# Kernel tuning notes

Hardware: AMD Instinct MI355X
Metric: run time of the kernel (lower is better)

## Reference

```python
import jax, jax.numpy as jnp
import numpy as np

N_NODES, N_GRAPHS, PER_GRAPH, N_EDGES = 20000, 200, 100, 320000
X_DIM, E_DIM, G_DIM = 32, 16, 32
NUM_EMB, HEADS, LAYERS = 64, 2, 3
EPS_GEN, EPS_LN = 1e-7, 1e-5


def _w(k, shape, scale=0.05):
    return (jax.random.normal(k, shape) * scale).astype(jnp.float32)


def _mlp3(x, W1, b1, W2, b2, W3, b3):
    h = jax.nn.leaky_relu(x @ W1 + b1)
    h = jax.nn.leaky_relu(h @ W2 + b2)
    return h @ W3 + b3


def _seg_sum(x, idx, n):
    return jax.ops.segment_sum(x, idx, num_segments=n)


def _seg_mean(x, idx, n):
    s = _seg_sum(x, idx, n)
    cnt = _seg_sum(jnp.ones((x.shape[0],), x.dtype), idx, n)
    return s / jnp.clip(cnt, 1.0, None)[:, None]


def _seg_softmax(logits, idx, n):
    # PyG softmax: subtract per-segment max, normalize with +1e-16
    m = jax.ops.segment_max(logits, idx, num_segments=n)
    m = jnp.where(jnp.isfinite(m), m, 0.0)
    e = jnp.exp(logits - m[idx])
    s = jax.ops.segment_sum(e, idx, num_segments=n)
    return e / (s[idx] + 1e-16)


def _graph_layernorm(x, batch, n_graphs):
    # PyG LayerNorm(mode='graph', affine=False): mean/var over all node-feature
    # entries of each graph.
    f = x.shape[-1]
    cnt = _seg_sum(jnp.ones((x.shape[0],), x.dtype), batch, n_graphs)
    norm = jnp.clip(cnt, 1.0, None) * f
    mean = _seg_sum(x.sum(-1), batch, n_graphs) / norm
    xc = x - mean[batch][:, None]
    var = _seg_sum((xc * xc).sum(-1), batch, n_graphs) / norm
    return xc / jnp.sqrt(var + EPS_LN)[batch][:, None]


def _forward(x, edge_attr, cond, edge_index, batch,
             x2h_W1, x2h_b1, x2h_W2, x2h_b2, x2h_W3, x2h_b3,
             e2h_W1, e2h_b1, e2h_W2, e2h_b2, e2h_W3, e2h_b3,
             c2h_W1, c2h_b1, c2h_W2, c2h_b2, c2h_W3, c2h_b3,
             gen_W, tr_Wq, tr_bq, tr_Wk, tr_bk, tr_Wv, tr_bv, tr_We, tr_Ws, tr_bs,
             lin_W, lin_b, ff_W1, ff_b1, ff_W2, ff_b2):
    N = x.shape[0]
    G = cond.shape[0]
    Naug = N + G
    o = _mlp3(x, x2h_W1, x2h_b1, x2h_W2, x2h_b2, x2h_W3, x2h_b3)
    e = _mlp3(edge_attr, e2h_W1, e2h_b1, e2h_W2, e2h_b2, e2h_W3, e2h_b3)
    c = _mlp3(cond, c2h_W1, c2h_b1, c2h_W2, c2h_b2, c2h_W3, c2h_b3)
    # virtual-node edges: node<->virtual node of its graph (virtual ids = N..N+G-1)
    u = jnp.arange(N, dtype=edge_index.dtype)
    v = batch.astype(edge_index.dtype) + N
    aug_ei = jnp.concatenate([edge_index, jnp.stack([u, v]), jnp.stack([v, u])], axis=1)
    e_p = jnp.zeros((2 * N, NUM_EMB), o.dtype).at[:, 0].set(1.0)
    aug_e = jnp.concatenate([e, e_p], axis=0)
    # add_self_loops(fill_value='mean'): self-loop attr = mean of incoming edge attrs
    loop_attr = _seg_mean(aug_e, aug_ei[1], Naug)
    loops = jnp.arange(Naug, dtype=edge_index.dtype)
    aug_ei = jnp.concatenate([aug_ei, jnp.stack([loops, loops])], axis=1)
    aug_e = jnp.concatenate([aug_e, loop_attr], axis=0)
    aug_batch = jnp.concatenate([batch, jnp.arange(G, dtype=batch.dtype)])
    o = jnp.concatenate([o, c], axis=0)  # [Naug, emb]
    src, dst = aug_ei[0], aug_ei[1]
    scale = 1.0 / float(np.sqrt(NUM_EMB))
    for i in range(LAYERS):
        # GENConv(aggr='add', norm=None, num_layers=1): sum(relu(x_j+e)+eps) + x, then Linear
        msg = jax.nn.relu(o[src] + aug_e) + EPS_GEN
        agg = (_seg_sum(msg, dst, Naug) + o) @ gen_W[i]
        # TransformerConv(2*emb -> emb, heads, edge_dim=emb, concat=True)
        xin = jnp.concatenate([o, agg], axis=1)  # [Naug, 2*emb]
        q = (xin @ tr_Wq[i] + tr_bq[i]).reshape(Naug, HEADS, NUM_EMB)
        k = (xin @ tr_Wk[i] + tr_bk[i]).reshape(Naug, HEADS, NUM_EMB)
        vv = (xin @ tr_Wv[i] + tr_bv[i]).reshape(Naug, HEADS, NUM_EMB)
        eh = (aug_e @ tr_We[i]).reshape(-1, HEADS, NUM_EMB)  # [E, H, C]
        kj = k[src] + eh
        alpha = _seg_softmax(jnp.einsum('ehc,ehc->eh', q[dst], kj) * scale, dst, Naug)
        tout = _seg_sum((vv[src] + eh) * alpha[..., None], dst, Naug)
        tout = tout.reshape(Naug, HEADS * NUM_EMB) + xin @ tr_Ws[i] + tr_bs[i]
        # residual + graph LayerNorm, then FFN + graph LayerNorm
        o = _graph_layernorm(o + tout @ lin_W[i] + lin_b[i], aug_batch, G)
        ff = jax.nn.leaky_relu(o @ ff_W1[i] + ff_b1[i]) @ ff_W2[i] + ff_b2[i]
        o = _graph_layernorm(o + ff, aug_batch, G)
    node_o, virt = o[:N], o[N:]
    glob = jnp.concatenate([_seg_mean(node_o, batch, G), virt, c], axis=1)
    o_final = jnp.concatenate([node_o, c[batch]], axis=1)
    return (o_final, glob)


def setup_inputs() -> dict:
    key = jax.random.key(0)
    ks = iter(jax.random.split(key, 64))
    inp = {}
    inp['x'] = jax.random.normal(next(ks), (N_NODES, X_DIM), dtype=jnp.float32)
    inp['edge_attr'] = jax.random.normal(next(ks), (N_EDGES, E_DIM), dtype=jnp.float32)
    inp['cond'] = jax.random.normal(next(ks), (N_GRAPHS, G_DIM), dtype=jnp.float32)
    src = jax.random.randint(next(ks), (N_EDGES,), 0, N_NODES)
    dst = (src // PER_GRAPH) * PER_GRAPH + jax.random.randint(next(ks), (N_EDGES,), 0, PER_GRAPH)
    inp['edge_index'] = jnp.stack([src, dst]).astype(jnp.int32)
    inp['batch'] = jnp.repeat(jnp.arange(N_GRAPHS, dtype=jnp.int32), PER_GRAPH)
    for p, nin in [('x2h', X_DIM), ('e2h', E_DIM), ('c2h', G_DIM)]:
        inp[p + '_W1'] = _w(next(ks), (nin, NUM_EMB)); inp[p + '_b1'] = _w(next(ks), (NUM_EMB,))
        inp[p + '_W2'] = _w(next(ks), (NUM_EMB, NUM_EMB)); inp[p + '_b2'] = _w(next(ks), (NUM_EMB,))
        inp[p + '_W3'] = _w(next(ks), (NUM_EMB, NUM_EMB)); inp[p + '_b3'] = _w(next(ks), (NUM_EMB,))
    HC = HEADS * NUM_EMB
    inp['gen_W'] = _w(next(ks), (LAYERS, NUM_EMB, NUM_EMB))
    inp['tr_Wq'] = _w(next(ks), (LAYERS, 2 * NUM_EMB, HC)); inp['tr_bq'] = _w(next(ks), (LAYERS, HC))
    inp['tr_Wk'] = _w(next(ks), (LAYERS, 2 * NUM_EMB, HC)); inp['tr_bk'] = _w(next(ks), (LAYERS, HC))
    inp['tr_Wv'] = _w(next(ks), (LAYERS, 2 * NUM_EMB, HC)); inp['tr_bv'] = _w(next(ks), (LAYERS, HC))
    inp['tr_We'] = _w(next(ks), (LAYERS, NUM_EMB, HC))
    inp['tr_Ws'] = _w(next(ks), (LAYERS, 2 * NUM_EMB, HC)); inp['tr_bs'] = _w(next(ks), (LAYERS, HC))
    inp['lin_W'] = _w(next(ks), (LAYERS, HC, NUM_EMB)); inp['lin_b'] = _w(next(ks), (LAYERS, NUM_EMB))
    inp['ff_W1'] = _w(next(ks), (LAYERS, NUM_EMB, 4 * NUM_EMB)); inp['ff_b1'] = _w(next(ks), (LAYERS, 4 * NUM_EMB))
    inp['ff_W2'] = _w(next(ks), (LAYERS, 4 * NUM_EMB, NUM_EMB)); inp['ff_b2'] = _w(next(ks), (LAYERS, NUM_EMB))
    return inp


def reference(x, edge_attr, cond, edge_index, batch,
              x2h_W1, x2h_b1, x2h_W2, x2h_b2, x2h_W3, x2h_b3,
              e2h_W1, e2h_b1, e2h_W2, e2h_b2, e2h_W3, e2h_b3,
              c2h_W1, c2h_b1, c2h_W2, c2h_b2, c2h_W3, c2h_b3,
              gen_W, tr_Wq, tr_bq, tr_Wk, tr_bk, tr_Wv, tr_bv, tr_We, tr_Ws, tr_bs,
              lin_W, lin_b, ff_W1, ff_b1, ff_W2, ff_b2):
    return _forward(x, edge_attr, cond, edge_index, batch,
                    x2h_W1, x2h_b1, x2h_W2, x2h_b2, x2h_W3, x2h_b3,
                    e2h_W1, e2h_b1, e2h_W2, e2h_b2, e2h_W3, e2h_b3,
                    c2h_W1, c2h_b1, c2h_W2, c2h_b2, c2h_W3, c2h_b3,
                    gen_W, tr_Wq, tr_bq, tr_Wk, tr_bk, tr_Wv, tr_bv, tr_We, tr_Ws, tr_bs,
                    lin_W, lin_b, ff_W1, ff_b1, ff_W2, ff_b2)
```

## Files before the change

kernel.cpp:

```cpp
#include <hip/hip_runtime.h>
#include <cstddef>

#define NN   20000
#define NG   200
#define NE   320000
#define NAUG 20200
#define NE2  360000
#define EAUG 380200
#define DD   64
#define HC   128

typedef float  f32x4 __attribute__((ext_vector_type(4)));
typedef short  s16x8 __attribute__((ext_vector_type(8)));

static __device__ __forceinline__ unsigned short bf16r(float f){
  unsigned u = __float_as_uint(f);
  u += 0x7FFFu + ((u >> 16) & 1u);
  return (unsigned short)(u >> 16);
}
static __device__ __forceinline__ float4 b2f4(ushort4 u){
  return make_float4(__uint_as_float((unsigned)u.x << 16),
                     __uint_as_float((unsigned)u.y << 16),
                     __uint_as_float((unsigned)u.z << 16),
                     __uint_as_float((unsigned)u.w << 16));
}
static __device__ __forceinline__ float d4(float4 a, float4 b){
  return a.x*b.x + a.y*b.y + a.z*b.z + a.w*b.w;
}
static __device__ __forceinline__ float4 f4ab(float4 a, float s, float4 b, float t){
  return make_float4(a.x*s + b.x*t, a.y*s + b.y*t, a.z*s + b.z*t, a.w*s + b.w*t);
}
static __device__ __forceinline__ float4 f4s(float4 a, float s){
  return make_float4(a.x*s, a.y*s, a.z*s, a.w*s);
}

#define WTAB_INIT { \
  {0,0,128,128,136,128,0},{0,0,128,128,136,128,16384},{0,0,128,128,136,128,32768}, \
  {1,0,128,128,136,128,0},{1,0,128,128,136,128,16384},{1,0,128,128,136,128,32768}, \
  {2,0,128,128,136,128,0},{2,0,128,128,136,128,16384},{2,0,128,128,136,128,32768}, \
  {3,0,128,128,136,128,0},{3,0,128,128,136,128,16384},{3,0,128,128,136,128,32768}, \
  {4,0,64,64,72,64,0},{4,0,64,64,72,64,4096},{4,0,64,64,72,64,8192}, \
  {5,0,128,64,136,64,0},{5,0,128,64,136,64,8192},{5,0,128,64,136,64,16384}, \
  {6,0,64,256,72,256,0},{6,0,64,256,72,256,16384},{6,0,64,256,72,256,32768}, \
  {7,0,256,64,264,64,0},{7,0,256,64,264,64,16384},{7,0,256,64,264,64,32768}, \
  {8,1,64,64,72,128,0},{8,1,64,64,72,128,64},{8,1,64,64,72,128,8192},{8,1,64,64,72,128,8256},{8,1,64,64,72,128,16384},{8,1,64,64,72,128,16448}, \
  {8,0,64,64,72,128,0},{8,0,64,64,72,128,64},{8,0,64,64,72,128,8192},{8,0,64,64,72,128,8256},{8,0,64,64,72,128,16384},{8,0,64,64,72,128,16448}, \
  {9,0,32,64,40,64,0},{10,0,64,64,72,64,0},{11,0,64,64,72,64,0}, \
  {12,0,16,64,40,64,0},{13,0,64,64,72,64,0},{14,0,64,64,72,64,0}, \
  {15,0,32,64,40,64,0},{16,0,64,64,72,64,0},{17,0,64,64,72,64,0} }

static const int WTAB_H[45][7] = WTAB_INIT;
__device__ static const int WTAB_D[45][7] = WTAB_INIT;

struct WPtrs { const float* p[18]; };

__global__ void wconv_all_k(WPtrs wp, unsigned short* __restrict__ outbase){
  int b = blockIdx.x;
// ... 30 lines not shown
                            const float* __restrict__ bias, int act,
                            const float* __restrict__ res, const float* __restrict__ res2,
                            int rstride, float* __restrict__ out, int ostride){
  extern __shared__ unsigned short smem[];
  const int KC  = (K > 128) ? 128 : K;
  const int KPc = KC + 8;
  const int KP  = K + 8;
  unsigned short* Wts  = smem;
  unsigned short* Asub = smem + NT*KPc;
  const int tid = threadIdx.x;
  const int wid = tid >> 6, lane = tid & 63;
  const int lrow = lane & 15, quad = lane >> 4;
  const int m0 = blockIdx.x * 64;
  f32x4 acc[NT/16];
  #pragma unroll
  for (int t = 0; t < NT/16; t++) acc[t] = (f32x4){0.f,0.f,0.f,0.f};

  for (int k0 = 0; k0 < K; k0 += KC){
    const int wv = NT*KPc/8, wrow = KPc/8;
    for (int i = tid; i < wv; i += 256){
      int n = i / wrow, c8 = i % wrow;
      *(uint4*)&Wts[n*KPc + c8*8] = *(const uint4*)&WtG[(size_t)n*KP + k0 + c8*8];
    }
    const int av = 64*KC/4, arow = KC/4;
    for (int i = tid; i < av; i += 256){
      int r = i / arow, c4i = i % arow;
      int m = m0 + r, k = k0 + c4i*4;
      float4 v = make_float4(0.f,0.f,0.f,0.f);
      if (m < M){
        v = *(const float4*)(A + (size_t)m*lda + k);
        if (A2){ float4 w = *(const float4*)(A2 + (size_t)m*lda + k);
                 v.x += w.x; v.y += w.y; v.z += w.z; v.w += w.w; }
      }
      ushort4 s; s.x = bf16r(v.x); s.y = bf16r(v.y); s.z = bf16r(v.z); s.w = bf16r(v.w);
      *(ushort4*)&Asub[r*KPc + c4i*4] = s;
    }
    __syncthreads();
    const int ksteps = KC >> 5;
    for (int ks = 0; ks < ksteps; ks++){
      s16x8 a = *(const s16x8*)&Asub[(wid*16 + lrow)*KPc + ks*32 + quad*8];
      #pragma unroll
      for (int nt = 0; nt < NT/16; nt++){
        s16x8 b = *(const s16x8*)&Wts[(nt*16 + lrow)*KPc + ks*32 + quad*8];
        acc[nt] = __builtin_amdgcn_mfma_f32_16x16x32_bf16(a, b, acc[nt], 0, 0, 0);
      }
    }
    __syncthreads();
  }

  const int mb = m0 + wid*16 + quad*4;
  #pragma unroll
  for (int nt = 0; nt < NT/16; nt++){
    int n = nt*16 + lrow;
    #pragma unroll
    for (int r = 0; r < 4; r++){
      int m = mb + r;
      if (m < M){
        float v = acc[nt][r];
        if (bias) v += bias[n];
        if (act)  v = v > 0.f ? v : 0.01f*v;
        if (res)  v += res [(size_t)m*rstride + n];
        if (res2) v += res2[(size_t)m*rstride + n];
        out[(size_t)m*ostride + n] = v;
      }
    }
  }
}

struct PW4 { const unsigned short* w[4]; const float* b[4]; };

__launch_bounds__(256)
__global__ void qkvs4_k(const float* __restrict__ A, int M, PW4 pw,
                        float* __restrict__ out){
  __shared__ __align__(16) unsigned short Wts[128*136];
  __shared__ __align__(16) unsigned short Asub[64*136];
  const unsigned short* WtG = pw.w[blockIdx.y];
  const float* bias = pw.b[blockIdx.y];
  const int tid = threadIdx.x;
  const int wid = tid >> 6, lane = tid & 63;
  const int lrow = lane & 15, quad = lane >> 4;
  const int m0 = blockIdx.x * 64;
  for (int i = tid; i < 128*17; i += 256){
    int n = i/17, c8 = i%17;
    *(uint4*)&Wts[n*136 + c8*8] = *(const uint4*)&WtG[(size_t)n*136 + c8*8];
  }
  for (int i = tid; i < 64*32; i += 256){
    int r = i >> 5, c4 = (i & 31)*4;
    int m = m0 + r;
    float4 v = make_float4(0.f,0.f,0.f,0.f);
    if (m < M) v = *(const float4*)(A + (size_t)m*128 + c4);
    ushort4 s; s.x=bf16r(v.x); s.y=bf16r(v.y); s.z=bf16r(v.z); s.w=bf16r(v.w);
    *(ushort4*)&Asub[r*136 + c4] = s;
  }
  __syncthreads();
  f32x4 acc[8];
  #pragma unroll
  for (int t=0;t<8;t++) acc[t] = (f32x4){0.f,0.f,0.f,0.f};
  #pragma unroll
  for (int ks = 0; ks < 4; ks++){
    s16x8 a = *(const s16x8*)&Asub[(wid*16 + lrow)*136 + ks*32 + quad*8];
    #pragma unroll
    for (int nt = 0; nt < 8; nt++){
      s16x8 b = *(const s16x8*)&Wts[(nt*16 + lrow)*136 + ks*32 + quad*8];
      acc[nt] = __builtin_amdgcn_mfma_f32_16x16x32_bf16(a, b, acc[nt], 0, 0, 0);
    }
  }
  const int mb = m0 + wid*16 + quad*4;
  const int yoff = blockIdx.y*128;
  #pragma unroll
  for (int nt = 0; nt < 8; nt++){
    int n = nt*16 + lrow;
    #pragma unroll
    for (int r = 0; r < 4; r++){
      int m = mb + r;
      if (m < M) out[(size_t)m*512 + yoff + n] = acc[nt][r] + bias[n];
    }
  }
}

struct PW2 { const unsigned short* w[2]; };

__launch_bounds__(256)
__global__ void qe2_k(const float* __restrict__ qkvs, int M, PW2 pw,
                      float* __restrict__ qe){
  __shared__ __align__(16) unsigned short Wts[64*72];
  __shared__ __align__(16) unsigned short Asub[64*72];
  const unsigned short* WtG = pw.w[blockIdx.y];
  const int tid = threadIdx.x;
  const int wid = tid >> 6, lane = tid & 63;
  const int lrow = lane & 15, quad = lane >> 4;
  const int m0 = blockIdx.x * 64;
  const int yoff = blockIdx.y * 64;
  for (int i = tid; i < 64*9; i += 256){
    int n = i/9, c8 = i%9;
    *(uint4*)&Wts[n*72 + c8*8] = *(const uint4*)&WtG[(size_t)n*72 + c8*8];
  }
  for (int i = tid; i < 64*16; i += 256){
    int r = i >> 4, c4 = (i & 15)*4;
    int m = m0 + r;
    float4 v = make_float4(0.f,0.f,0.f,0.f);
    if (m < M) v = *(const float4*)(qkvs + (size_t)m*512 + yoff + c4);
    ushort4 s; s.x=bf16r(v.x); s.y=bf16r(v.y); s.z=bf16r(v.z); s.w=bf16r(v.w);
    *(ushort4*)&Asub[r*72 + c4] = s;
  }
  __syncthreads();
  f32x4 acc[4];
  #pragma unroll
  for (int t=0;t<4;t++) acc[t] = (f32x4){0.f,0.f,0.f,0.f};
  #pragma unroll
  for (int ks = 0; ks < 2; ks++){
    s16x8 a = *(const s16x8*)&Asub[(wid*16 + lrow)*72 + ks*32 + quad*8];
    #pragma unroll
    for (int nt = 0; nt < 4; nt++){
      s16x8 b = *(const s16x8*)&Wts[(nt*16 + lrow)*72 + ks*32 + quad*8];
      acc[nt] = __builtin_amdgcn_mfma_f32_16x16x32_bf16(a, b, acc[nt], 0, 0, 0);
    }
  }
  const int mb = m0 + wid*16 + quad*4;
  #pragma unroll
  for (int nt = 0; nt < 4; nt++){
    int n = nt*16 + lrow;
    #pragma unroll
    for (int r = 0; r < 4; r++){
      int m = mb + r;
      if (m < M) qe[(size_t)m*HC + yoff + n] = acc[nt][r];
    }
  }
}

__launch_bounds__(256)
__global__ void tout2_k(const float* __restrict__ wv, int M, PW2 pw,
                        const float* __restrict__ t1, const float* __restrict__ qkvs,
                        float* __restrict__ tout){
  __shared__ __align__(16) unsigned short Wts[64*72];
  __shared__ __align__(16) unsigned short Asub[64*72];
  const unsigned short* WtG = pw.w[blockIdx.y];
  const int tid = threadIdx.x;
  const int wid = tid >> 6, lane = tid & 63;
  const int lrow = lane & 15, quad = lane >> 4;
  const int m0 = blockIdx.x * 64;
  const int yoff = blockIdx.y * 64;
  for (int i = tid; i < 64*9; i += 256){
    int n = i/9, c8 = i%9;
    *(uint4*)&Wts[n*72 + c8*8] = *(const uint4*)&WtG[(size_t)n*72 + c8*8];
  }
  for (int i = tid; i < 64*16; i += 256){
    int r = i >> 4, c4 = (i & 15)*4;
    int m = m0 + r;
    float4 v = make_float4(0.f,0.f,0.f,0.f);
    if (m < M) v = *(const float4*)(wv + (size_t)m*HC + yoff + c4);
    ushort4 s; s.x=bf16r(v.x); s.y=bf16r(v.y); s.z=bf16r(v.z); s.w=bf16r(v.w);
    *(ushort4*)&Asub[r*72 + c4] = s;
  }
  __syncthreads();
  f32x4 acc[4];
  #pragma unroll
  for (int t=0;t<4;t++) acc[t] = (f32x4){0.f,0.f,0.f,0.f};
  #pragma unroll
  for (int ks = 0; ks < 2; ks++){
    s16x8 a = *(const s16x8*)&Asub[(wid*16 + lrow)*72 + ks*32 + quad*8];
    #pragma unroll
    for (int nt = 0; nt < 4; nt++){
      s16x8 b = *(const s16x8*)&Wts[(nt*16 + lrow)*72 + ks*32 + quad*8];
      acc[nt] = __builtin_amdgcn_mfma_f32_16x16x32_bf16(a, b, acc[nt], 0, 0, 0);
    }
  }
  const int mb = m0 + wid*16 + quad*4;
  #pragma unroll
  for (int nt = 0; nt < 4; nt++){
    int n = nt*16 + lrow;
    #pragma unroll
    for (int r = 0; r < 4; r++){
      int m = mb + r;
      if (m < M)
        tout[(size_t)m*HC + yoff + n] = acc[nt][r]
          + t1[(size_t)m*HC + yoff + n] + qkvs[(size_t)m*512 + 384 + yoff + n];
    }
  }
}

__launch_bounds__(256)
__global__ void mlp3_mfma_k(const float* __restrict__ X, int M, int Din,
                            const unsigned short* __restrict__ w1t,
                            const unsigned short* __restrict__ w2t,
                            const unsigned short* __restrict__ w3t,
                            const float* __restrict__ b1, const float* __restrict__ b2,
                            const float* __restrict__ b3,
                            const int* __restrict__ perm, float* __restrict__ out){
  __shared__ __align__(16) unsigned short W1s[64*40], W2s[64*72], W3s[64*72];
  __shared__ __align__(16) unsigned short xs[64*40], hs[64*72];
  __shared__ float bsh[192];
  const int tid = threadIdx.x;
  for (int i = tid; i < 320; i += 256)  *(uint4*)&W1s[i*8] = *(const uint4*)&w1t[i*8];
  for (int i = tid; i < 576; i += 256){ *(uint4*)&W2s[i*8] = *(const uint4*)&w2t[i*8];
                                        *(uint4*)&W3s[i*8] = *(const uint4*)&w3t[i*8]; }
  if (tid < 64){ bsh[tid] = b1[tid]; bsh[64+tid] = b2[tid]; bsh[128+tid] = b3[tid]; }
  const int m0 = blockIdx.x * 64;
  for (int i = tid; i < 512; i += 256){
    int r = i >> 3, c4 = (i & 7) * 4;
    int m = m0 + r;
    float4 v = make_float4(0.f,0.f,0.f,0.f);
    if (m < M && c4 < Din) v = *(const float4*)(X + (size_t)m*Din + c4);
    ushort4 s; s.x = bf16r(v.x); s.y = bf16r(v.y); s.z = bf16r(v.z); s.w = bf16r(v.w);
    *(ushort4*)&xs[r*40 + c4] = s;
  }
  __syncthreads();
  const int wid = tid >> 6, lane = tid & 63;
  const int lrow = lane & 15, quad = lane >> 4;
  f32x4 acc[4];

  #pragma unroll
  for (int t = 0; t < 4; t++) acc[t] = (f32x4){0.f,0.f,0.f,0.f};
  {
    s16x8 a = *(const s16x8*)&xs[(wid*16 + lrow)*40 + quad*8];
    #pragma unroll
    for (int nt = 0; nt < 4; nt++){
      s16x8 b = *(const s16x8*)&W1s[(nt*16 + lrow)*40 + quad*8];
      acc[nt] = __builtin_amdgcn_mfma_f32_16x16x32_bf16(a, b, acc[nt], 0, 0, 0);
    }
  }
  #pragma unroll
  for (int nt = 0; nt < 4; nt++){
    int n = nt*16 + lrow;
    #pragma unroll
    for (int r = 0; r < 4; r++){
      float v = acc[nt][r] + bsh[n];
      v = v > 0.f ? v : 0.01f*v;
      hs[(wid*16 + quad*4 + r)*72 + n] = bf16r(v);
    }
  }
  __syncthreads();

  #pragma unroll
  for (int t = 0; t < 4; t++) acc[t] = (f32x4){0.f,0.f,0.f,0.f};
  #pragma unroll
  for (int ks = 0; ks < 2; ks++){
    s16x8 a = *(const s16x8*)&hs[(wid*16 + lrow)*72 + ks*32 + quad*8];
// ... 5 lines not shown
  }
  __syncthreads();
  #pragma unroll
  for (int nt = 0; nt < 4; nt++){
    int n = nt*16 + lrow;
    #pragma unroll
    for (int r = 0; r < 4; r++){
      float v = acc[nt][r] + bsh[64 + n];
      v = v > 0.f ? v : 0.01f*v;
      hs[(wid*16 + quad*4 + r)*72 + n] = bf16r(v);
    }
  }
  __syncthreads();

  #pragma unroll
  for (int t = 0; t < 4; t++) acc[t] = (f32x4){0.f,0.f,0.f,0.f};
  #pragma unroll
  for (int ks = 0; ks < 2; ks++){
    s16x8 a = *(const s16x8*)&hs[(wid*16 + lrow)*72 + ks*32 + quad*8];
    #pragma unroll
    for (int nt = 0; nt < 4; nt++){
      s16x8 b = *(const s16x8*)&W3s[(nt*16 + lrow)*72 + ks*32 + quad*8];
      acc[nt] = __builtin_amdgcn_mfma_f32_16x16x32_bf16(a, b, acc[nt], 0, 0, 0);
    }
  }
  #pragma unroll
  for (int nt = 0; nt < 4; nt++){
    int n = nt*16 + lrow;
    #pragma unroll
    for (int r = 0; r < 4; r++){
      int m = m0 + wid*16 + quad*4 + r;
      if (m < M){
        int orow = perm ? perm[m] : m;
        out[(size_t)orow*64 + n] = acc[nt][r] + bsh[128 + n];
      }
    }
  }
}

__global__ void build_edges_k(const int* __restrict__ ei, const int* __restrict__ batch,
                              int* __restrict__ srcA, int* __restrict__ dstA){
  int idx = blockIdx.x*256 + threadIdx.x;
  if (idx >= EAUG) return;
  int s, d;
  if (idx < NE)          { s = ei[idx];              d = ei[NE+idx]; }
  else if (idx < NE+NN)  { int i = idx-NE;           s = i;            d = batch[i]+NN; }
  else if (idx < NE2)    { int i = idx-(NE+NN);      s = batch[i]+NN;  d = i; }
  else                   { int i = idx-NE2;          s = i;            d = i; }
  srcA[idx]=s; dstA[idx]=d;
}

__global__ void count_k(const int* __restrict__ dstA, int* __restrict__ cnt){
  int e = blockIdx.x*256 + threadIdx.x;
  if (e < EAUG) atomicAdd(&cnt[dstA[e]], 1);
}

__global__ void scan_k(const int* __restrict__ cnt, int* __restrict__ rowptr){
  __shared__ int part[1024];
  int tid = threadIdx.x;
  const int per = (NAUG + 1023) / 1024;
  int base = tid * per;
  int s = 0;
  for (int i=0;i<per;i++){ int idx=base+i; if (idx<NAUG) s += cnt[idx]; }
  part[tid] = s;
  __syncthreads();
  for (int off=1; off<1024; off<<=1){
    int v = (tid>=off) ? part[tid-off] : 0;
    __syncthreads();
    part[tid] += v;
    __syncthreads();
  }
  int run = (tid==0) ? 0 : part[tid-1];
  for (int i=0;i<per;i++){
    int idx=base+i;
    if (idx<NAUG){ rowptr[idx]=run; run += cnt[idx]; }
  }
  if (tid==0) rowptr[NAUG] = EAUG;
}

__global__ void scatter_k(const int* __restrict__ srcA, const int* __restrict__ dstA,
                          const int* __restrict__ rowptr, int* __restrict__ cursor,
                          int* __restrict__ eid, int* __restrict__ esrc,
                          int* __restrict__ epos){
  int e = blockIdx.x*256 + threadIdx.x;
  if (e >= EAUG) return;
  int d = dstA[e];
  int pos = rowptr[d] + atomicAdd(&cursor[d], 1);
  eid[pos]  = e;
  esrc[pos] = srcA[e];
  epos[e]   = pos;
}

__global__ void set_ep_k(const int* __restrict__ epos, float* __restrict__ aug_p){
  int idx = blockIdx.x*256 + threadIdx.x;
  if (idx >= 2*NN*DD) return;
  int i = idx >> 6, c = idx & 63;
  aug_p[(size_t)epos[NE + i]*DD + c] = (c==0) ? 1.f : 0.f;
}

__launch_bounds__(256)
__global__ void loopmean_k(const int* __restrict__ rowptr, const int* __restrict__ eid,
                           const int* __restrict__ epos, float* __restrict__ aug_p){
  int tid = threadIdx.x;
  int d = blockIdx.x*16 + (tid>>4);
  if (d >= NAUG) return;
  int t4 = (tid & 15)*4;
  int beg = rowptr[d], end = rowptr[d+1];
  float4 s = make_float4(0.f,0.f,0.f,0.f); int n = 0;
  for (int p=beg; p<end; p++){
    int e = eid[p];
    if (e < NE2){
      float4 a = *(const float4*)(aug_p + (size_t)p*DD + t4);
      s.x += a.x; s.y += a.y; s.z += a.z; s.w += a.w;
      n++;
    }
  }
  float cv = (n < 1) ? 1.f : (float)n;
  *(float4*)(aug_p + (size_t)epos[NE2+d]*DD + t4) = f4s(s, 1.f/cv);
}

__launch_bounds__(512)
__global__ void msg_graph_k(const float* __restrict__ o, const float* __restrict__ aug_p,
                            const int* __restrict__ rowptr,
                            const int* __restrict__ esrc, float* __restrict__ aggsum){
  __shared__ __align__(16) float OS[101*72];
  __shared__ unsigned char EL[3072];
  const int g = blockIdx.x >> 1, half = blockIdx.x & 1;
  const int tid = threadIdx.x;
  for (int i = tid; i < 101*16; i += 512){
    int ln = i >> 4, c4 = (i & 15)*4;
    int row = (ln < 100) ? g*100 + ln : NN + g;
    *(float4*)&OS[ln*72 + c4] = *(const float4*)(o + (size_t)row*DD + c4);
  }
  const int baseA = rowptr[g*100];
  const int lenA  = rowptr[g*100 + 100] - baseA;
  const int baseB = rowptr[NN + g];
  const int lenB  = rowptr[NN + g + 1] - baseB;
  const bool useL = (lenA + lenB) <= 3072;
  if (useL){
    for (int i = tid; i < lenA; i += 512){
      int s = esrc[baseA + i];
      EL[i] = (unsigned char)((s >= NN) ? 100 : (s - g*100));
    }
    for (int i = tid; i < lenB; i += 512){
      int s = esrc[baseB + i];
      EL[lenA + i] = (unsigned char)((s >= NN) ? 100 : (s - g*100));
    }
  }
  __syncthreads();
  const int gr = tid >> 4, t4 = (tid & 15)*4;
  const int ld0 = half ? 51 : 0, ld1 = half ? 101 : 51;
  for (int ld = ld0 + gr; ld < ld1; ld += 32){
    int d, pbeg, pend, eofs;
    if (ld < 100){ d = g*100 + ld; pbeg = rowptr[d]; pend = rowptr[d+1]; eofs = -baseA; }
    else         { d = NN + g;     pbeg = baseB;     pend = baseB + lenB; eofs = lenA - baseB; }
    float4 acc = make_float4(0.f,0.f,0.f,0.f);
    for (int p = pbeg; p < pend; p++){
      int ls;
      if (useL) ls = EL[p + eofs];
      else { int s = esrc[p]; ls = (s >= NN) ? 100 : (s - g*100); }
      float4 ov = *(const float4*)&OS[ls*72 + t4];
      float4 ae = *(const float4*)(aug_p + (size_t)p*DD + t4);
      acc.x += fmaxf(ov.x+ae.x, 0.f) + 1e-7f;
      acc.y += fmaxf(ov.y+ae.y, 0.f) + 1e-7f;
      acc.z += fmaxf(ov.z+ae.z, 0.f) + 1e-7f;
      acc.w += fmaxf(ov.w+ae.w, 0.f) + 1e-7f;
    }
    *(float4*)(aggsum + (size_t)d*DD + t4) = acc;
  }
}

__global__ void copy_o_xin_k(const float* __restrict__ o, float* __restrict__ xin){
  int idx = blockIdx.x*256 + threadIdx.x;
  if (idx >= NAUG*DD) return;
  int n = idx >> 6, c = idx & 63;
  xin[(size_t)n*HC + c] = o[idx];
}

__launch_bounds__(512)
__global__ void attn_graph_k(const float* __restrict__ qkvs, const float* __restrict__ qe,
                             const float* __restrict__ aug_p,
                             const int* __restrict__ rowptr,
                             const int* __restrict__ esrc,
                             float* __restrict__ t1, float* __restrict__ wbuf){
  __shared__ __align__(16) unsigned short KV[101*264];
  __shared__ unsigned char EL[3072];
  const int g = blockIdx.x >> 1, half = blockIdx.x & 1;
  const int tid = threadIdx.x;
  for (int i = tid; i < 101*64; i += 512){
    int ln = i >> 6, c4 = (i & 63)*4;
    int row = (ln < 100) ? g*100 + ln : NN + g;
    float4 v = *(const float4*)(qkvs + (size_t)row*512 + 128 + c4);
    ushort4 s; s.x=bf16r(v.x); s.y=bf16r(v.y); s.z=bf16r(v.z); s.w=bf16r(v.w);
    *(ushort4*)&KV[ln*264 + c4] = s;
  }
  const int baseA = rowptr[g*100];
  const int lenA  = rowptr[g*100 + 100] - baseA;
  const int baseB = rowptr[NN + g];
  const int lenB  = rowptr[NN + g + 1] - baseB;
  const bool useL = (lenA + lenB) <= 3072;
  if (useL){
    for (int i = tid; i < lenA; i += 512){
      int s = esrc[baseA + i];
      EL[i] = (unsigned char)((s >= NN) ? 100 : (s - g*100));
    }
    for (int i = tid; i < lenB; i += 512){
      int s = esrc[baseB + i];
      EL[lenA + i] = (unsigned char)((s >= NN) ? 100 : (s - g*100));
    }
  }
  __syncthreads();
  const int gr = tid >> 4, t4 = (tid & 15)*4;
  const int ld0 = half ? 51 : 0, ld1 = half ? 101 : 51;
  for (int ld = ld0 + gr; ld < ld1; ld += 32){
    int d, pbeg, pend, eofs;
    if (ld < 100){ d = g*100 + ld; pbeg = rowptr[d]; pend = rowptr[d+1]; eofs = -baseA; }
    else         { d = NN + g;     pbeg = baseB;     pend = baseB + lenB; eofs = lenA - baseB; }
    const float* qr = qkvs + (size_t)d*512;
    float4 q0  = *(const float4*)(qr + t4);
    float4 q1  = *(const float4*)(qr + 64 + t4);
    float4 qe0 = *(const float4*)(qe + (size_t)d*HC + t4);
    float4 qe1 = *(const float4*)(qe + (size_t)d*HC + 64 + t4);
    float m0=-1e30f, m1=-1e30f, l0=0.f, l1=0.f;
    float4 a0 = make_float4(0.f,0.f,0.f,0.f), a1 = a0, w0 = a0, w1 = a0;
    for (int p = pbeg; p < pend; p++){
      int ls;
      if (useL) ls = EL[p + eofs];
      else { int s = esrc[p]; ls = (s >= NN) ? 100 : (s - g*100); }
      const unsigned short* kr = &KV[ls*264];
      float4 k0 = b2f4(*(const ushort4*)(kr + t4));
      float4 k1 = b2f4(*(const ushort4*)(kr + 64 + t4));
      float4 v0 = b2f4(*(const ushort4*)(kr + 128 + t4));
      float4 v1 = b2f4(*(const ushort4*)(kr + 192 + t4));
      float4 ae = *(const float4*)(aug_p + (size_t)p*DD + t4);
      float p0 = d4(q0,k0) + d4(qe0,ae);
      float p1 = d4(q1,k1) + d4(qe1,ae);
      p0 += __shfl_xor(p0,8); p0 += __shfl_xor(p0,4); p0 += __shfl_xor(p0,2); p0 += __shfl_xor(p0,1);
      p1 += __shfl_xor(p1,8); p1 += __shfl_xor(p1,4); p1 += __shfl_xor(p1,2); p1 += __shfl_xor(p1,1);
      p0 *= 0.125f; p1 *= 0.125f;
      float nm0 = fmaxf(m0, p0);
      float sc0 = __expf(m0 - nm0);
      float e0  = __expf(p0 - nm0);
      l0 = l0*sc0 + e0; a0 = f4ab(a0, sc0, v0, e0); w0 = f4ab(w0, sc0, ae, e0); m0 = nm0;
      float nm1 = fmaxf(m1, p1);
      float sc1 = __expf(m1 - nm1);
      float e1  = __expf(p1 - nm1);
      l1 = l1*sc1 + e1; a1 = f4ab(a1, sc1, v1, e1); w1 = f4ab(w1, sc1, ae, e1); m1 = nm1;
    }
    float i0 = 1.f/(l0 + 1e-16f), i1 = 1.f/(l1 + 1e-16f);
    *(float4*)(t1   + (size_t)d*HC + t4)      = f4s(a0, i0);
    *(float4*)(t1   + (size_t)d*HC + 64 + t4) = f4s(a1, i1);
    *(float4*)(wbuf + (size_t)d*HC + t4)      = f4s(w0, i0);
    *(float4*)(wbuf + (size_t)d*HC + 64 + t4) = f4s(w1, i1);
  }
}

__global__ void ln_k(const float* __restrict__ y, float* __restrict__ o){
  int g = blockIdx.x, tid = threadIdx.x;
  float sum=0.f, ss=0.f;
  for (int i=tid; i<101*64; i+=256){
    int nd=i>>6, c=i&63;
    int row = (nd<100) ? g*100+nd : NN+g;
    float v = y[(size_t)row*DD + c];
    sum += v; ss += v*v;
  }
  #pragma unroll
  for (int off=32; off; off>>=1){ sum += __shfl_xor(sum, off); ss += __shfl_xor(ss, off); }
  __shared__ float s1[4], s2[4];
  if ((tid&63)==0){ s1[tid>>6]=sum; s2[tid>>6]=ss; }
  __syncthreads();
  sum = s1[0]+s1[1]+s1[2]+s1[3];
  ss  = s2[0]+s2[1]+s2[2]+s2[3];
  const float inv = 1.f/6464.f;
  float mean = sum*inv;
  float var  = ss*inv - mean*mean;
  float rstd = rsqrtf(var + 1e-5f);
  for (int i=tid; i<101*64; i+=256){
    int nd=i>>6, c=i&63;
    int row = (nd<100) ? g*100+nd : NN+g;
    o[(size_t)row*DD + c] = (y[(size_t)row*DD + c] - mean)*rstd;
  }
}

__global__ void copy_c_o_k(const float* __restrict__ c_emb, float* __restrict__ o){
  int idx = blockIdx.x*256 + threadIdx.x;
  if (idx >= NG*DD) return;
  o[(size_t)NN*DD + idx] = c_emb[idx];
// ... 44 lines not shown
  const int*   edge_index= (const int*)  d_in[3];
  const int*   batch     = (const int*)  d_in[4];
  const float* xW1=(const float*)d_in[5],  *xb1=(const float*)d_in[6],
             * xW2=(const float*)d_in[7],  *xb2=(const float*)d_in[8],
             * xW3=(const float*)d_in[9],  *xb3=(const float*)d_in[10];
  const float* eW1=(const float*)d_in[11], *eb1=(const float*)d_in[12],
             * eW2=(const float*)d_in[13], *eb2=(const float*)d_in[14],
             * eW3=(const float*)d_in[15], *eb3=(const float*)d_in[16];
  const float* cW1=(const float*)d_in[17], *cb1=(const float*)d_in[18],
             * cW2=(const float*)d_in[19], *cb2=(const float*)d_in[20],
             * cW3=(const float*)d_in[21], *cb3=(const float*)d_in[22];
  const float* gen_W=(const float*)d_in[23];
  const float* trWq=(const float*)d_in[24], *trbq=(const float*)d_in[25];
  const float* trWk=(const float*)d_in[26], *trbk=(const float*)d_in[27];
  const float* trWv=(const float*)d_in[28], *trbv=(const float*)d_in[29];
  const float* trWe=(const float*)d_in[30];
  const float* trWs=(const float*)d_in[31], *trbs=(const float*)d_in[32];
  const float* linW=(const float*)d_in[33], *linb=(const float*)d_in[34];
  const float* ffW1=(const float*)d_in[35], *ffb1=(const float*)d_in[36];
  const float* ffW2=(const float*)d_in[37], *ffb2=(const float*)d_in[38];
  float* out = (float*)d_out;

  float* ws = (float*)d_ws;
  size_t off = 0;
  auto alloc = [&](size_t n)->float*{ float* p = ws + off; off += (n + 63) & ~(size_t)63; return p; };
  int*      srcA  = (int*)alloc(EAUG);
  int*      dstA  = (int*)alloc(EAUG);
  int*      cnt   = (int*)alloc(NAUG);
  int*      rowptr= (int*)alloc(NAUG+1);
  int*      cursor= (int*)alloc(NAUG);
  int*      eid   = (int*)alloc(EAUG);
  int*      esrc  = (int*)alloc(EAUG);
  int*      epos  = (int*)alloc(EAUG);
  float*    aug_p = alloc((size_t)EAUG*DD);
  float*    o     = alloc((size_t)NAUG*DD);
  float*    c_emb = alloc((size_t)NG*DD);
  float*    ybuf  = alloc((size_t)NAUG*DD);
  float*    aggsum= alloc((size_t)NAUG*DD);
  float*    xin   = alloc((size_t)NAUG*HC);
  float*    xqkvs = alloc((size_t)NAUG*512);
  float*    qeb   = alloc((size_t)NAUG*HC);
  float*    toutb = alloc((size_t)NAUG*HC);
  float*    t1    = alloc((size_t)NAUG*HC);
  float*    wbuf  = alloc((size_t)NAUG*HC);
  float*    ffh   = alloc((size_t)NAUG*256);
  unsigned short* warena = (unsigned short*)alloc(222720);
  if (off*sizeof(float) > ws_size) return;

  const unsigned short* wptr[45];
  int wblk = 0;
  { size_t woff = 0;
    for (int j = 0; j < 45; j++){
      wptr[j] = warena + woff;
      int e = WTAB_H[j][3]*WTAB_H[j][4];
      woff += (size_t)e;
      wblk += cdiv(e, 256);
    } }

  WPtrs wp;
  wp.p[0]=trWq; wp.p[1]=trWk; wp.p[2]=trWv; wp.p[3]=trWs; wp.p[4]=gen_W;
  wp.p[5]=linW; wp.p[6]=ffW1; wp.p[7]=ffW2; wp.p[8]=trWe;
  wp.p[9]=xW1; wp.p[10]=xW2; wp.p[11]=xW3;
  wp.p[12]=eW1; wp.p[13]=eW2; wp.p[14]=eW3;
  wp.p[15]=cW1; wp.p[16]=cW2; wp.p[17]=cW3;
  wconv_all_k<<<wblk,256,0,stream>>>(wp, warena);

  build_edges_k<<<cdiv(EAUG,256),256,0,stream>>>(edge_index, batch, srcA, dstA);
  hipMemsetAsync(cnt, 0, sizeof(int)*NAUG, stream);
  hipMemsetAsync(cursor, 0, sizeof(int)*NAUG, stream);
  count_k<<<cdiv(EAUG,256),256,0,stream>>>(dstA, cnt);
  scan_k<<<1,1024,0,stream>>>(cnt, rowptr);
  scatter_k<<<cdiv(EAUG,256),256,0,stream>>>(srcA, dstA, rowptr, cursor, eid, esrc, epos);

  mlp3_mfma_k<<<cdiv(NN,64),256,0,stream>>>(x,        NN, 32, wptr[36],wptr[37],wptr[38], xb1,xb2,xb3, nullptr, o);
  mlp3_mfma_k<<<cdiv(NG,64),256,0,stream>>>(cond,     NG, 32, wptr[42],wptr[43],wptr[44], cb1,cb2,cb3, nullptr, c_emb);
  mlp3_mfma_k<<<cdiv(NE,64),256,0,stream>>>(edge_attr,NE, 16, wptr[39],wptr[40],wptr[41], eb1,eb2,eb3, epos, aug_p);
  set_ep_k<<<cdiv(2*NN*DD,256),256,0,stream>>>(epos, aug_p);
  loopmean_k<<<cdiv(NAUG,16),256,0,stream>>>(rowptr, eid, epos, aug_p);
  copy_c_o_k<<<cdiv(NG*DD,256),256,0,stream>>>(c_emb, o);

  for (int L=0; L<3; L++){
    const float* lb_i = linb + (size_t)L*DD;
    const float* f1b  = ffb1 + (size_t)L*256;
    const float* f2b  = ffb2 + (size_t)L*DD;
    const unsigned short* genT = wptr[12+L], *linT = wptr[15+L], *ff1T = wptr[18+L], *ff2T = wptr[21+L];
    PW4 pw4; pw4.w[0]=wptr[0+L]; pw4.w[1]=wptr[3+L]; pw4.w[2]=wptr[6+L]; pw4.w[3]=wptr[9+L];
    pw4.b[0]=trbq+(size_t)L*HC; pw4.b[1]=trbk+(size_t)L*HC;
    pw4.b[2]=trbv+(size_t)L*HC; pw4.b[3]=trbs+(size_t)L*HC;
    PW2 pwE; pwE.w[0]=wptr[24+2*L]; pwE.w[1]=wptr[25+2*L];
    PW2 pwT; pwT.w[0]=wptr[30+2*L]; pwT.w[1]=wptr[31+2*L];

    msg_graph_k<<<2*NG,512,0,stream>>>(o, aug_p, rowptr, esrc, aggsum);
    copy_o_xin_k<<<cdiv(NAUG*DD,256),256,0,stream>>>(o, xin);
    gemm_mfma( 64, aggsum, o, NAUG, 64, 64, genT, nullptr, 0, nullptr, nullptr, 0, xin+64, HC, stream);
    qkvs4_k<<<dim3(cdiv(NAUG,64),4),256,0,stream>>>(xin, NAUG, pw4, xqkvs);
    qe2_k<<<dim3(cdiv(NAUG,64),2),256,0,stream>>>(xqkvs, NAUG, pwE, qeb);
    attn_graph_k<<<2*NG,512,0,stream>>>(xqkvs, qeb, aug_p, rowptr, esrc, t1, wbuf);
    tout2_k<<<dim3(cdiv(NAUG,64),2),256,0,stream>>>(wbuf, NAUG, pwT, t1, xqkvs, toutb);
    gemm_mfma( 64, toutb, nullptr, NAUG, 128, 128, linT, lb_i, 0, o, nullptr, DD, ybuf, DD, stream);
    ln_k<<<NG,256,0,stream>>>(ybuf, o);
    gemm_mfma(256, o,   nullptr, NAUG,  64,  64, ff1T, f1b, 1, nullptr, nullptr, 0, ffh, 256, stream);
    gemm_mfma( 64, ffh, nullptr, NAUG, 256, 256, ff2T, f2b, 0, o, nullptr, DD, ybuf, DD, stream);
    ln_k<<<NG,256,0,stream>>>(ybuf, o);
  }

  glob_k<<<NG,64,0,stream>>>(o, c_emb, out + (size_t)NN*HC);
  ofinal_k<<<cdiv(NN*HC,256),256,0,stream>>>(o, c_emb, batch, out);
}
```

Measured before the change: 1.289 ms.

## Store edge embeddings as bf16 and split attention into score, aggregate, weight-sum kernels

```diff
diff --git a/kernel.cpp b/kernel.cpp
--- a/kernel.cpp
+++ b/kernel.cpp
@@ -23,6 +23,9 @@
                      __uint_as_float((unsigned)u.y << 16),
                      __uint_as_float((unsigned)u.z << 16),
                      __uint_as_float((unsigned)u.w << 16));
+}
+static __device__ __forceinline__ ushort4 f2b4(float4 v){
+  ushort4 s; s.x=bf16r(v.x); s.y=bf16r(v.y); s.z=bf16r(v.z); s.w=bf16r(v.w); return s;
 }
 static __device__ __forceinline__ float d4(float4 a, float4 b){
   return a.x*b.x + a.y*b.y + a.z*b.z + a.w*b.w;
@@ -119,8 +122,7 @@
         if (A2){ float4 w = *(const float4*)(A2 + (size_t)m*lda + k);
                  v.x += w.x; v.y += w.y; v.z += w.z; v.w += w.w; }
       }
-      ushort4 s; s.x = bf16r(v.x); s.y = bf16r(v.y); s.z = bf16r(v.z); s.w = bf16r(v.w);
-      *(ushort4*)&Asub[r*KPc + c4i*4] = s;
+      *(ushort4*)&Asub[r*KPc + c4i*4] = f2b4(v);
     }
     __syncthreads();
     const int ksteps = KC >> 5;
@@ -176,8 +178,7 @@
     int m = m0 + r;
     float4 v = make_float4(0.f,0.f,0.f,0.f);
     if (m < M) v = *(const float4*)(A + (size_t)m*128 + c4);
-    ushort4 s; s.x=bf16r(v.x); s.y=bf16r(v.y); s.z=bf16r(v.z); s.w=bf16r(v.w);
-    *(ushort4*)&Asub[r*136 + c4] = s;
+    *(ushort4*)&Asub[r*136 + c4] = f2b4(v);
   }
   __syncthreads();
   f32x4 acc[8];
@@ -227,8 +228,7 @@
     int m = m0 + r;
     float4 v = make_float4(0.f,0.f,0.f,0.f);
     if (m < M) v = *(const float4*)(qkvs + (size_t)m*512 + yoff + c4);
-    ushort4 s; s.x=bf16r(v.x); s.y=bf16r(v.y); s.z=bf16r(v.z); s.w=bf16r(v.w);
-    *(ushort4*)&Asub[r*72 + c4] = s;
+    *(ushort4*)&Asub[r*72 + c4] = f2b4(v);
   }
   __syncthreads();
   f32x4 acc[4];
@@ -276,8 +276,7 @@
     int m = m0 + r;
     float4 v = make_float4(0.f,0.f,0.f,0.f);
     if (m < M) v = *(const float4*)(wv + (size_t)m*HC + yoff + c4);
-    ushort4 s; s.x=bf16r(v.x); s.y=bf16r(v.y); s.z=bf16r(v.z); s.w=bf16r(v.w);
-    *(ushort4*)&Asub[r*72 + c4] = s;
+    *(ushort4*)&Asub[r*72 + c4] = f2b4(v);
   }
   __syncthreads();
   f32x4 acc[4];
@@ -313,7 +312,8 @@
                             const unsigned short* __restrict__ w3t,
                             const float* __restrict__ b1, const float* __restrict__ b2,
                             const float* __restrict__ b3,
-                            const int* __restrict__ perm, float* __restrict__ out){
+                            const int* __restrict__ perm, float* __restrict__ out,
+                            unsigned short* __restrict__ outb){
   __shared__ __align__(16) unsigned short W1s[64*40], W2s[64*72], W3s[64*72];
   __shared__ __align__(16) unsigned short xs[64*40], hs[64*72];
   __shared__ float bsh[192];
@@ -328,8 +328,7 @@
     int m = m0 + r;
     float4 v = make_float4(0.f,0.f,0.f,0.f);
     if (m < M && c4 < Din) v = *(const float4*)(X + (size_t)m*Din + c4);
-    ushort4 s; s.x = bf16r(v.x); s.y = bf16r(v.y); s.z = bf16r(v.z); s.w = bf16r(v.w);
-    *(ushort4*)&xs[r*40 + c4] = s;
+    *(ushort4*)&xs[r*40 + c4] = f2b4(v);
   }
   __syncthreads();
   const int wid = tid >> 6, lane = tid & 63;
@@ -401,7 +400,9 @@
       int m = m0 + wid*16 + quad*4 + r;
       if (m < M){
         int orow = perm ? perm[m] : m;
-        out[(size_t)orow*64 + n] = acc[nt][r] + bsh[128 + n];
+        float v = acc[nt][r] + bsh[128 + n];
+        if (outb) outb[(size_t)orow*64 + n] = bf16r(v);
+        else      out [(size_t)orow*64 + n] = v;
       }
     }
   }
@@ -450,26 +451,27 @@
 __global__ void scatter_k(const int* __restrict__ srcA, const int* __restrict__ dstA,
                           const int* __restrict__ rowptr, int* __restrict__ cursor,
                           int* __restrict__ eid, int* __restrict__ esrc,
-                          int* __restrict__ epos){
+                          int* __restrict__ epos, int* __restrict__ pdst){
   int e = blockIdx.x*256 + threadIdx.x;
   if (e >= EAUG) return;
   int d = dstA[e];
   int pos = rowptr[d] + atomicAdd(&cursor[d], 1);
   eid[pos]  = e;
   esrc[pos] = srcA[e];
+  pdst[pos] = d;
   epos[e]   = pos;
 }
 
-__global__ void set_ep_k(const int* __restrict__ epos, float* __restrict__ aug_p){
+__global__ void set_ep_k(const int* __restrict__ epos, unsigned short* __restrict__ aug_b){
   int idx = blockIdx.x*256 + threadIdx.x;
   if (idx >= 2*NN*DD) return;
   int i = idx >> 6, c = idx & 63;
-  aug_p[(size_t)epos[NE + i]*DD + c] = (c==0) ? 1.f : 0.f;
+  aug_b[(size_t)epos[NE + i]*DD + c] = (c==0) ? (unsigned short)0x3F80 : (unsigned short)0;
 }
 
 __launch_bounds__(256)
 __global__ void loopmean_k(const int* __restrict__ rowptr, const int* __restrict__ eid,
-                           const int* __restrict__ epos, float* __restrict__ aug_p){
+                           const int* __restrict__ epos, unsigned short* __restrict__ aug_b){
   int tid = threadIdx.x;
   int d = blockIdx.x*16 + (tid>>4);
   if (d >= NAUG) return;
@@ -479,17 +481,17 @@
   for (int p=beg; p<end; p++){
     int e = eid[p];
     if (e < NE2){
-      float4 a = *(const float4*)(aug_p + (size_t)p*DD + t4);
+      float4 a = b2f4(*(const ushort4*)(aug_b + (size_t)p*DD + t4));
       s.x += a.x; s.y += a.y; s.z += a.z; s.w += a.w;
       n++;
     }
   }
   float cv = (n < 1) ? 1.f : (float)n;
-  *(float4*)(aug_p + (size_t)epos[NE2+d]*DD + t4) = f4s(s, 1.f/cv);
+  *(ushort4*)(aug_b + (size_t)epos[NE2+d]*DD + t4) = f2b4(f4s(s, 1.f/cv));
 }
 
 __launch_bounds__(512)
-__global__ void msg_graph_k(const float* __restrict__ o, const float* __restrict__ aug_p,
+__global__ void msg_graph_k(const float* __restrict__ o, const unsigned short* __restrict__ aug_b,
                             const int* __restrict__ rowptr,
                             const int* __restrict__ esrc, float* __restrict__ aggsum){
   __shared__ __align__(16) float OS[101*72];
@@ -529,7 +531,7 @@
       if (useL) ls = EL[p + eofs];
       else { int s = esrc[p]; ls = (s >= NN) ? 100 : (s - g*100); }
       float4 ov = *(const float4*)&OS[ls*72 + t4];
-      float4 ae = *(const float4*)(aug_p + (size_t)p*DD + t4);
+      float4 ae = b2f4(*(const ushort4*)(aug_b + (size_t)p*DD + t4));
       acc.x += fmaxf(ov.x+ae.x, 0.f) + 1e-7f;
       acc.y += fmaxf(ov.y+ae.y, 0.f) + 1e-7f;
       acc.z += fmaxf(ov.z+ae.z, 0.f) + 1e-7f;
@@ -547,21 +549,44 @@
 }
 
 __launch_bounds__(512)
-__global__ void attn_graph_k(const float* __restrict__ qkvs, const float* __restrict__ qe,
-                             const float* __restrict__ aug_p,
-                             const int* __restrict__ rowptr,
-                             const int* __restrict__ esrc,
-                             float* __restrict__ t1, float* __restrict__ wbuf){
-  __shared__ __align__(16) unsigned short KV[101*264];
+__global__ void scoredot_k(const float* __restrict__ qkvs, const float* __restrict__ qe,
+                           const unsigned short* __restrict__ aug_b,
+                           const int* __restrict__ pdst, const int* __restrict__ esrc,
+                           float2* __restrict__ lg){
+  int p = blockIdx.x*32 + (threadIdx.x >> 4);
+  if (p >= EAUG) return;
+  int t4 = (threadIdx.x & 15)*4;
+  int d = pdst[p], s = esrc[p];
+  const float* qr = qkvs + (size_t)d*512;
+  const float* kr = qkvs + (size_t)s*512 + 128;
+  float4 q0  = *(const float4*)(qr + t4);
+  float4 q1  = *(const float4*)(qr + 64 + t4);
+  float4 qe0 = *(const float4*)(qe + (size_t)d*HC + t4);
+  float4 qe1 = *(const float4*)(qe + (size_t)d*HC + 64 + t4);
+  float4 k0  = *(const float4*)(kr + t4);
+  float4 k1  = *(const float4*)(kr + 64 + t4);
+  float4 ae  = b2f4(*(const ushort4*)(aug_b + (size_t)p*DD + t4));
+  float p0 = d4(q0,k0) + d4(qe0,ae);
+  float p1 = d4(q1,k1) + d4(qe1,ae);
+  p0 += __shfl_xor(p0,8); p0 += __shfl_xor(p0,4); p0 += __shfl_xor(p0,2); p0 += __shfl_xor(p0,1);
+  p1 += __shfl_xor(p1,8); p1 += __shfl_xor(p1,4); p1 += __shfl_xor(p1,2); p1 += __shfl_xor(p1,1);
+  if ((threadIdx.x & 15) == 0) lg[p] = make_float2(p0*0.125f, p1*0.125f);
+}
+
+__launch_bounds__(512)
+__global__ void attn_lite_k(const float* __restrict__ qkvs, const float2* __restrict__ lg,
+                            const int* __restrict__ rowptr, const int* __restrict__ esrc,
+                            float* __restrict__ t1, float2* __restrict__ m2,
+                            float2* __restrict__ linv2){
+  __shared__ __align__(16) unsigned short VS[101*128];
   __shared__ unsigned char EL[3072];
   const int g = blockIdx.x >> 1, half = blockIdx.x & 1;
   const int tid = threadIdx.x;
-  for (int i = tid; i < 101*64; i += 512){
-    int ln = i >> 6, c4 = (i & 63)*4;
+  for (int i = tid; i < 101*32; i += 512){
+    int ln = i >> 5, c4 = (i & 31)*4;
     int row = (ln < 100) ? g*100 + ln : NN + g;
-    float4 v = *(const float4*)(qkvs + (size_t)row*512 + 128 + c4);
-    ushort4 s; s.x=bf16r(v.x); s.y=bf16r(v.y); s.z=bf16r(v.z); s.w=bf16r(v.w);
-    *(ushort4*)&KV[ln*264 + c4] = s;
+    float4 v = *(const float4*)(qkvs + (size_t)row*512 + 256 + c4);
+    *(ushort4*)&VS[ln*128 + c4] = f2b4(v);
   }
   const int baseA = rowptr[g*100];
   const int lenA  = rowptr[g*100 + 100] - baseA;
@@ -585,43 +610,58 @@
     int d, pbeg, pend, eofs;
     if (ld < 100){ d = g*100 + ld; pbeg = rowptr[d]; pend = rowptr[d+1]; eofs = -baseA; }
     else         { d = NN + g;     pbeg = baseB;     pend = baseB + lenB; eofs = lenA - baseB; }
-    const float* qr = qkvs + (size_t)d*512;
-    float4 q0  = *(const float4*)(qr + t4);
-    float4 q1  = *(const float4*)(qr + 64 + t4);
-    float4 qe0 = *(const float4*)(qe + (size_t)d*HC + t4);
-    float4 qe1 = *(const float4*)(qe + (size_t)d*HC + 64 + t4);
     float m0=-1e30f, m1=-1e30f, l0=0.f, l1=0.f;
-    float4 a0 = make_float4(0.f,0.f,0.f,0.f), a1 = a0, w0 = a0, w1 = a0;
+    float4 a0 = make_float4(0.f,0.f,0.f,0.f), a1 = a0;
+    float2 lv = lg[pbeg];
     for (int p = pbeg; p < pend; p++){
+      float2 nxt = (p+1 < pend) ? lg[p+1] : make_float2(0.f,0.f);
       int ls;
       if (useL) ls = EL[p + eofs];
       else { int s = esrc[p]; ls = (s >= NN) ? 100 : (s - g*100); }
-      const unsigned short* kr = &KV[ls*264];
-      float4 k0 = b2f4(*(const ushort4*)(kr + t4));
-      float4 k1 = b2f4(*(const ushort4*)(kr + 64 + t4));
-      float4 v0 = b2f4(*(const ushort4*)(kr + 128 + t4));
-      float4 v1 = b2f4(*(const ushort4*)(kr + 192 + t4));
-      float4 ae = *(const float4*)(aug_p + (size_t)p*DD + t4);
-      float p0 = d4(q0,k0) + d4(qe0,ae);
-      float p1 = d4(q1,k1) + d4(qe1,ae);
-      p0 += __shfl_xor(p0,8); p0 += __shfl_xor(p0,4); p0 += __shfl_xor(p0,2); p0 += __shfl_xor(p0,1);
-      p1 += __shfl_xor(p1,8); p1 += __shfl_xor(p1,4); p1 += __shfl_xor(p1,2); p1 += __shfl_xor(p1,1);
-      p0 *= 0.125f; p1 *= 0.125f;
-      float nm0 = fmaxf(m0, p0);
+      const unsigned short* vr = &VS[ls*128];
+      float4 v0 = b2f4(*(const ushort4*)(vr + t4));
+      float4 v1 = b2f4(*(const ushort4*)(vr + 64 + t4));
+      float nm0 = fmaxf(m0, lv.x);
       float sc0 = __expf(m0 - nm0);
-      float e0  = __expf(p0 - nm0);
-      l0 = l0*sc0 + e0; a0 = f4ab(a0, sc0, v0, e0); w0 = f4ab(w0, sc0, ae, e0); m0 = nm0;
-      float nm1 = fmaxf(m1, p1);
+      float e0  = __expf(lv.x - nm0);
+      l0 = l0*sc0 + e0; a0 = f4ab(a0, sc0, v0, e0); m0 = nm0;
+      float nm1 = fmaxf(m1, lv.y);
       float sc1 = __expf(m1 - nm1);
-      float e1  = __expf(p1 - nm1);
-      l1 = l1*sc1 + e1; a1 = f4ab(a1, sc1, v1, e1); w1 = f4ab(w1, sc1, ae, e1); m1 = nm1;
+      float e1  = __expf(lv.y - nm1);
+      l1 = l1*sc1 + e1; a1 = f4ab(a1, sc1, v1, e1); m1 = nm1;
+      lv = nxt;
     }
     float i0 = 1.f/(l0 + 1e-16f), i1 = 1.f/(l1 + 1e-16f);
-    *(float4*)(t1   + (size_t)d*HC + t4)      = f4s(a0, i0);
-    *(float4*)(t1   + (size_t)d*HC + 64 + t4) = f4s(a1, i1);
-    *(float4*)(wbuf + (size_t)d*HC + t4)      = f4s(w0, i0);
-    *(float4*)(wbuf + (size_t)d*HC + 64 + t4) = f4s(w1, i1);
-  }
+    *(float4*)(t1 + (size_t)d*HC + t4)      = f4s(a0, i0);
+    *(float4*)(t1 + (size_t)d*HC + 64 + t4) = f4s(a1, i1);
+    if ((tid & 15) == 0){
+      m2[d]    = make_float2(m0, m1);
+      linv2[d] = make_float2(i0, i1);
+    }
+  }
+}
+
+__launch_bounds__(256)
+__global__ void wsum_k(const unsigned short* __restrict__ aug_b, const float2* __restrict__ lg,
+                       const float2* __restrict__ m2, const float2* __restrict__ linv2,
+                       const int* __restrict__ rowptr, float* __restrict__ wbuf){
+  int tid = threadIdx.x;
+  int d = blockIdx.x*16 + (tid>>4);
+  if (d >= NAUG) return;
+  int t4 = (tid & 15)*4;
+  float2 m = m2[d], li = linv2[d];
+  float4 w0 = make_float4(0.f,0.f,0.f,0.f), w1 = w0;
+  int beg = rowptr[d], end = rowptr[d+1];
+  for (int p = beg; p < end; p++){
+    float2 lv = lg[p];
+    float4 ae = b2f4(*(const ushort4*)(aug_b + (size_t)p*DD + t4));
+    float a0 = __expf(lv.x - m.x) * li.x;
+    float a1 = __expf(lv.y - m.y) * li.y;
+    w0.x += a0*ae.x; w0.y += a0*ae.y; w0.z += a0*ae.z; w0.w += a0*ae.w;
+    w1.x += a1*ae.x; w1.y += a1*ae.y; w1.z += a1*ae.z; w1.w += a1*ae.w;
+  }
+  *(float4*)(wbuf + (size_t)d*HC + t4)      = w0;
+  *(float4*)(wbuf + (size_t)d*HC + 64 + t4) = w1;
 }
 
 __global__ void ln_k(const float* __restrict__ y, float* __restrict__ o){
@@ -732,7 +772,8 @@
   int*      eid   = (int*)alloc(EAUG);
   int*      esrc  = (int*)alloc(EAUG);
   int*      epos  = (int*)alloc(EAUG);
-  float*    aug_p = alloc((size_t)EAUG*DD);
+  int*      pdst  = (int*)alloc(EAUG);
+  unsigned short* aug_b = (unsigned short*)alloc((size_t)EAUG*DD/2);
   float*    o     = alloc((size_t)NAUG*DD);
   float*    c_emb = alloc((size_t)NG*DD);
   float*    ybuf  = alloc((size_t)NAUG*DD);
@@ -744,6 +785,9 @@
   float*    t1    = alloc((size_t)NAUG*HC);
   float*    wbuf  = alloc((size_t)NAUG*HC);
   float*    ffh   = alloc((size_t)NAUG*256);
+  float2*   lgb   = (float2*)alloc((size_t)EAUG*2);
+  float2*   m2v   = (float2*)alloc((size_t)NAUG*2);
+  float2*   li2v  = (float2*)alloc((size_t)NAUG*2);
   unsigned short* warena = (unsigned short*)alloc(222720);
   if (off*sizeof(float) > ws_size) return;
 
@@ -770,13 +814,13 @@
   hipMemsetAsync(cursor, 0, sizeof(int)*NAUG, stream);
   count_k<<<cdiv(EAUG,256),256,0,stream>>>(dstA, cnt);
   scan_k<<<1,1024,0,stream>>>(cnt, rowptr);
-  scatter_k<<<cdiv(EAUG,256),256,0,stream>>>(srcA, dstA, rowptr, cursor, eid, esrc, epos);
-
-  mlp3_mfma_k<<<cdiv(NN,64),256,0,stream>>>(x,        NN, 32, wptr[36],wptr[37],wptr[38], xb1,xb2,xb3, nullptr, o);
-  mlp3_mfma_k<<<cdiv(NG,64),256,0,stream>>>(cond,     NG, 32, wptr[42],wptr[43],wptr[44], cb1,cb2,cb3, nullptr, c_emb);
-  mlp3_mfma_k<<<cdiv(NE,64),256,0,stream>>>(edge_attr,NE, 16, wptr[39],wptr[40],wptr[41], eb1,eb2,eb3, epos, aug_p);
-  set_ep_k<<<cdiv(2*NN*DD,256),256,0,stream>>>(epos, aug_p);
-  loopmean_k<<<cdiv(NAUG,16),256,0,stream>>>(rowptr, eid, epos, aug_p);
+  scatter_k<<<cdiv(EAUG,256),256,0,stream>>>(srcA, dstA, rowptr, cursor, eid, esrc, epos, pdst);
+
+  mlp3_mfma_k<<<cdiv(NN,64),256,0,stream>>>(x,        NN, 32, wptr[36],wptr[37],wptr[38], xb1,xb2,xb3, nullptr, o,     nullptr);
+  mlp3_mfma_k<<<cdiv(NG,64),256,0,stream>>>(cond,     NG, 32, wptr[42],wptr[43],wptr[44], cb1,cb2,cb3, nullptr, c_emb, nullptr);
+  mlp3_mfma_k<<<cdiv(NE,64),256,0,stream>>>(edge_attr,NE, 16, wptr[39],wptr[40],wptr[41], eb1,eb2,eb3, epos,    nullptr, aug_b);
+  set_ep_k<<<cdiv(2*NN*DD,256),256,0,stream>>>(epos, aug_b);
+  loopmean_k<<<cdiv(NAUG,16),256,0,stream>>>(rowptr, eid, epos, aug_b);
   copy_c_o_k<<<cdiv(NG*DD,256),256,0,stream>>>(c_emb, o);
 
   for (int L=0; L<3; L++){
@@ -790,12 +834,14 @@
     PW2 pwE; pwE.w[0]=wptr[24+2*L]; pwE.w[1]=wptr[25+2*L];
     PW2 pwT; pwT.w[0]=wptr[30+2*L]; pwT.w[1]=wptr[31+2*L];
 
-    msg_graph_k<<<2*NG,512,0,stream>>>(o, aug_p, rowptr, esrc, aggsum);
+    msg_graph_k<<<2*NG,512,0,stream>>>(o, aug_b, rowptr, esrc, aggsum);
     copy_o_xin_k<<<cdiv(NAUG*DD,256),256,0,stream>>>(o, xin);
     gemm_mfma( 64, aggsum, o, NAUG, 64, 64, genT, nullptr, 0, nullptr, nullptr, 0, xin+64, HC, stream);
     qkvs4_k<<<dim3(cdiv(NAUG,64),4),256,0,stream>>>(xin, NAUG, pw4, xqkvs);
     qe2_k<<<dim3(cdiv(NAUG,64),2),256,0,stream>>>(xqkvs, NAUG, pwE, qeb);
-    attn_graph_k<<<2*NG,512,0,stream>>>(xqkvs, qeb, aug_p, rowptr, esrc, t1, wbuf);
+    scoredot_k<<<cdiv(EAUG,32),512,0,stream>>>(xqkvs, qeb, aug_b, pdst, esrc, lgb);
+    attn_lite_k<<<2*NG,512,0,stream>>>(xqkvs, lgb, rowptr, esrc, t1, m2v, li2v);
+    wsum_k<<<cdiv(NAUG,16),256,0,stream>>>(aug_b, lgb, m2v, li2v, rowptr, wbuf);
     tout2_k<<<dim3(cdiv(NAUG,64),2),256,0,stream>>>(wbuf, NAUG, pwT, t1, xqkvs, toutb);
     gemm_mfma( 64, toutb, nullptr, NAUG, 128, 128, linT, lb_i, 0, o, nullptr, DD, ybuf, DD, stream);
     ln_k<<<NG,256,0,stream>>>(ybuf, o);
```

After: 1.338 ms. 1.04x slower.
